# Optimization experiments

Hardware: AMD Instinct MI355X
Metric: run time of the kernel (lower is better)

The kernel has to match this reference:

```python
import jax, jax.numpy as jnp
import numpy as np

N = 50000          # num nodes
DEG = 16           # fixed degree (uniform CSR)
E = N * DEG        # num edges
R = 8              # num relations
IN = 128
HID = 128
OUT = 40
BN_EPS = 1e-5


def setup_inputs() -> dict:
    key = jax.random.key(0)
    k = jax.random.split(key, 5)
    x = jax.random.normal(k[0], (N, IN), jnp.float32)
    # glorot-ish init for per-relation weights
    W1 = jax.random.normal(k[1], (R, IN, HID), jnp.float32) * (2.0 / (IN + HID)) ** 0.5
    W2 = jax.random.normal(k[2], (R, HID, OUT), jnp.float32) * (2.0 / (HID + OUT)) ** 0.5
    ptr = jnp.arange(N + 1, dtype=jnp.int32) * DEG            # CSR row offsets
    idx = jax.random.randint(k[3], (E,), 0, N, jnp.int32)     # neighbor (src) ids
    edge_types = jax.random.randint(k[4], (E,), 0, R, jnp.int32)
    return {
        "x": x, "W1": W1, "W2": W2,
        "bn_gamma": jnp.ones((HID,), jnp.float32),
        "bn_beta": jnp.zeros((HID,), jnp.float32),
        "bn_mean": jnp.zeros((HID,), jnp.float32),
        "bn_var": jnp.ones((HID,), jnp.float32),
        "ptr": ptr, "idx": idx, "edge_types": edge_types,
    }


def _rgcn_layer(h, W, ptr, idx, edge_types):
    # RGCNOP: out[i] = sum_{e in [ptr[i],ptr[i+1])} x[idx[e]] @ W[etype[e]]
    # Efficient form: transform every node by every relation once, then gather
    # the (src, etype) pair per edge and scatter-add into destinations.
    xr = jnp.einsum('nd,rdh->nrh', h, W)             # [N, R, H]
    msgs = xr[idx, edge_types]                       # [E, H] irregular gather
    deg = ptr[1:] - ptr[:-1]                         # [N]
    dst = jnp.repeat(jnp.arange(ptr.shape[0] - 1, dtype=jnp.int32), deg,
                     total_repeat_length=idx.shape[0])
    agg = jax.ops.segment_sum(msgs, dst, num_segments=ptr.shape[0] - 1)
    return agg / deg[:, None].astype(agg.dtype)      # degree normalization


def reference(x, W1, W2, bn_gamma, bn_beta, bn_mean, bn_var, ptr, idx, edge_types):
    h = _rgcn_layer(x, W1, ptr, idx, edge_types)
    # BatchNorm1d in eval mode (history_size=0, dropout inactive)
    h = (h - bn_mean) * jax.lax.rsqrt(bn_var + BN_EPS) * bn_gamma + bn_beta
    h = jax.nn.relu(h)
    h = _rgcn_layer(h, W2, ptr, idx, edge_types)
    return jax.nn.log_softmax(h, axis=-1)
```

## Files before the change

### kernel.cpp

```cpp
#include <hip/hip_runtime.h>
#include <math.h>

typedef __attribute__((ext_vector_type(8))) short bf16x8;
typedef __attribute__((ext_vector_type(4))) float f32x4;

constexpr int kN   = 50000;
constexpr int kR   = 8;
constexpr int kIn  = 128;
constexpr int kHid = 128;
constexpr int kOut = 40;
constexpr int kNT  = 16;
constexpr int kLds = 1032;
constexpr float kBnEps = 1e-5f;

__device__ inline ushort f2bf(float x) {
    uint u = __float_as_uint(x);
    u += 0x7FFFu + ((u >> 16) & 1u);
    return (ushort)(u >> 16);
}
__device__ inline float bf2f(ushort s) { return __uint_as_float(((uint)s) << 16); }

__device__ __forceinline__ void pack_unit(const float* __restrict__ W,
                                          ushort* __restrict__ dst,
                                          int N, int frag, int lane)
{
    const int kt = frag & 31;
    const int nt = frag >> 5;
    const int n  = nt * 16 + (lane & 15);
    const int q  = lane >> 4;
    ushort hv[8];
    #pragma unroll
    for (int j = 0; j < 8; ++j) {
        const int k = kt * 32 + q * 8 + j;
        hv[j] = f2bf((n < N) ? W[(size_t)k * N + n] : 0.f);
    }
    const size_t o = ((size_t)frag * 64 + lane) * 8;
    *(ushort4*)&dst[o]     = make_ushort4(hv[0], hv[1], hv[2], hv[3]);
    *(ushort4*)&dst[o + 4] = make_ushort4(hv[4], hv[5], hv[6], hv[7]);
}

__global__ __launch_bounds__(256)
void prep(const float* __restrict__ x,  ushort* __restrict__ xb,
          const float* __restrict__ W1, ushort* __restrict__ W1hi,
          const float* __restrict__ W2, ushort* __restrict__ W2hi)
{
    const int b   = blockIdx.x;
    const int tid = threadIdx.x;
    if (b < 3125) {
        const size_t i = ((size_t)b * 256 + tid) * 8;
        const float4 v0 = *(const float4*)&x[i];
        const float4 v1 = *(const float4*)&x[i + 4];
        *(ushort4*)&xb[i]     = make_ushort4(f2bf(v0.x), f2bf(v0.y), f2bf(v0.z), f2bf(v0.w));
        *(ushort4*)&xb[i + 4] = make_ushort4(f2bf(v1.x), f2bf(v1.y), f2bf(v1.z), f2bf(v1.w));
    } else if (b < 3125 + 64) {
        pack_unit(W1, W1hi, kHid, (b - 3125) * 4 + (tid >> 6), tid & 63);
    } else {
        const int frag = (b - 3189) * 4 + (tid >> 6);
        if (frag < 96) pack_unit(W2, W2hi, kOut, frag, tid & 63);
    }
}

#define ACCUM_ET(ET, VX, VY)                                   \
    if      ((ET) == 0) { a0.x += (VX); a0.y += (VY); }        \
    else if ((ET) == 1) { a1.x += (VX); a1.y += (VY); }        \
    else if ((ET) == 2) { a2.x += (VX); a2.y += (VY); }        \
    else if ((ET) == 3) { a3.x += (VX); a3.y += (VY); }        \
    else if ((ET) == 4) { a4.x += (VX); a4.y += (VY); }        \
    else if ((ET) == 5) { a5.x += (VX); a5.y += (VY); }        \
    else if ((ET) == 6) { a6.x += (VX); a6.y += (VY); }        \
    else                { a7.x += (VX); a7.y += (VY); }

#define GATHER(BV, SRC) \
    const ushort2 BV = *(const ushort2*)&feat[(size_t)(SRC) * 128 + d2];

#define ACCUM_EDGE(J, BV) \
    { const int et = __builtin_amdgcn_readlane(ve, J); ACCUM_ET(et, bf2f(BV.x), bf2f(BV.y)) }

#define STORE_AGG(RR, AV) \
    *(ushort2*)&aggHi[n][(RR) * 128 + d2] = make_ushort2(f2bf(AV.x), f2bf(AV.y));

__device__ __forceinline__ void phaseA_bf16(const ushort* __restrict__ feat,
                                            const int* __restrict__ ptr,
                                            const int* __restrict__ idx,
                                            const int* __restrict__ etype,
                                            int base, ushort (*aggHi)[kLds])
{
    const int lane = threadIdx.x & 63;
    const int wid  = threadIdx.x >> 6;
    const int d2   = lane * 2;

    #pragma unroll
    for (int t = 0; t < 2; ++t) {
        const int n    = wid * 2 + t;
        const int node = base + n;
        const int p0   = ptr[node];
        const int deg  = ptr[node + 1] - p0;

        float2 a0 = {0.f,0.f}, a1 = {0.f,0.f}, a2 = {0.f,0.f}, a3 = {0.f,0.f};
        float2 a4 = {0.f,0.f}, a5 = {0.f,0.f}, a6 = {0.f,0.f}, a7 = {0.f,0.f};

        if (deg == 16) {
            const int vi = idx[p0 + (lane & 15)];
            const int ve = etype[p0 + (lane & 15)];
            const int s0  = __builtin_amdgcn_readlane(vi, 0);
            const int s1  = __builtin_amdgcn_readlane(vi, 1);
            const int s2  = __builtin_amdgcn_readlane(vi, 2);
            const int s3  = __builtin_amdgcn_readlane(vi, 3);
            const int s4  = __builtin_amdgcn_readlane(vi, 4);
            const int s5  = __builtin_amdgcn_readlane(vi, 5);
            const int s6  = __builtin_amdgcn_readlane(vi, 6);
            const int s7  = __builtin_amdgcn_readlane(vi, 7);
            const int s8  = __builtin_amdgcn_readlane(vi, 8);
            const int s9  = __builtin_amdgcn_readlane(vi, 9);
            const int s10 = __builtin_amdgcn_readlane(vi, 10);
            const int s11 = __builtin_amdgcn_readlane(vi, 11);
            const int s12 = __builtin_amdgcn_readlane(vi, 12);
            const int s13 = __builtin_amdgcn_readlane(vi, 13);
            const int s14 = __builtin_amdgcn_readlane(vi, 14);
            const int s15 = __builtin_amdgcn_readlane(vi, 15);
            GATHER(b0,  s0)  GATHER(b1,  s1)  GATHER(b2,  s2)  GATHER(b3,  s3)
            GATHER(b4,  s4)  GATHER(b5,  s5)  GATHER(b6,  s6)  GATHER(b7,  s7)
            GATHER(b8,  s8)  GATHER(b9,  s9)  GATHER(b10, s10) GATHER(b11, s11)
            GATHER(b12, s12) GATHER(b13, s13) GATHER(b14, s14) GATHER(b15, s15)
            ACCUM_EDGE(0,  b0)  ACCUM_EDGE(1,  b1)  ACCUM_EDGE(2,  b2)  ACCUM_EDGE(3,  b3)
            ACCUM_EDGE(4,  b4)  ACCUM_EDGE(5,  b5)  ACCUM_EDGE(6,  b6)  ACCUM_EDGE(7,  b7)
            ACCUM_EDGE(8,  b8)  ACCUM_EDGE(9,  b9)  ACCUM_EDGE(10, b10) ACCUM_EDGE(11, b11)
            ACCUM_EDGE(12, b12) ACCUM_EDGE(13, b13) ACCUM_EDGE(14, b14) ACCUM_EDGE(15, b15)
        } else {
            for (int e = p0; e < p0 + deg; ++e) {
                const int src = __builtin_amdgcn_readfirstlane(idx[e]);
                const int et  = __builtin_amdgcn_readfirstlane(etype[e]);
                const ushort2 u = *(const ushort2*)&feat[(size_t)src * 128 + d2];
                ACCUM_ET(et, bf2f(u.x), bf2f(u.y))
            }
        }
        STORE_AGG(0, a0) STORE_AGG(1, a1) STORE_AGG(2, a2) STORE_AGG(3, a3)
        STORE_AGG(4, a4) STORE_AGG(5, a5) STORE_AGG(6, a6) STORE_AGG(7, a7)
    }
}

__global__ __launch_bounds__(512, 4)
void rgcn_layer1(const ushort* __restrict__ xb,
                 const ushort* __restrict__ W1hi,
                 const float* __restrict__ gamma, const float* __restrict__ beta,
                 const float* __restrict__ mean,  const float* __restrict__ var,
                 const int* __restrict__ ptr, const int* __restrict__ idx,
                 const int* __restrict__ etype,
                 ushort* __restrict__ h1b)
{
    __shared__ ushort aggHi[kNT][kLds];
    const int tid  = threadIdx.x;
    const int base = blockIdx.x * kNT;

    phaseA_bf16(xb, ptr, idx, etype, base, aggHi);
    __syncthreads();

    const int lane = tid & 63;
    const int wid  = tid >> 6;
    const int m    = lane & 15;
    const int q    = lane >> 4;

    const bf16x8* Bh = (const bf16x8*)W1hi + (size_t)wid * 32 * 64 + lane;
    f32x4 acc = {0.f, 0.f, 0.f, 0.f};

    #pragma unroll 4
    for (int kt = 0; kt < 32; ++kt) {
        const bf16x8 ah = *(const bf16x8*)&aggHi[m][kt * 32 + q * 8];
        const bf16x8 bh = Bh[(size_t)kt * 64];
        acc = __builtin_amdgcn_mfma_f32_16x16x32_bf16(ah, bh, acc, 0, 0, 0);
    }

    const int c = wid * 16 + m;
    const float g  = gamma[c] * rsqrtf(var[c] + kBnEps);
    const float mu = mean[c];
    const float bt = beta[c];
    #pragma unroll
    for (int i = 0; i < 4; ++i) {
        const int node = base + q * 4 + i;
        const float invdeg = 1.0f / (float)(ptr[node + 1] - ptr[node]);
        float v = (acc[i] * invdeg - mu) * g + bt;
        v = fmaxf(v, 0.f);
        h1b[(size_t)node * kHid + c] = f2bf(v);
    }
}

__global__ __launch_bounds__(512, 4)
void rgcn_layer2(const ushort* __restrict__ h1b,
                 const ushort* __restrict__ W2hi,
                 const int* __restrict__ ptr, const int* __restrict__ idx,
                 const int* __restrict__ etype,
                 float* __restrict__ out)
{
    __shared__ ushort aggHi[kNT][kLds];
    __shared__ float logits[kNT][48];
    const int tid  = threadIdx.x;
    const int base = blockIdx.x * kNT;

    phaseA_bf16(h1b, ptr, idx, etype, base, aggHi);
    __syncthreads();

    const int lane = tid & 63;
    const int wid  = tid >> 6;
    const int m    = lane & 15;
    const int q    = lane >> 4;

    if (wid < 3) {
        const bf16x8* Bh = (const bf16x8*)W2hi + (size_t)wid * 32 * 64 + lane;
        f32x4 acc = {0.f, 0.f, 0.f, 0.f};
        #pragma unroll 4
        for (int kt = 0; kt < 32; ++kt) {
            const bf16x8 ah = *(const bf16x8*)&aggHi[m][kt * 32 + q * 8];
            const bf16x8 bh = Bh[(size_t)kt * 64];
            acc = __builtin_amdgcn_mfma_f32_16x16x32_bf16(ah, bh, acc, 0, 0, 0);
        }
        const int n = wid * 16 + m;
        if (n < kOut) {
            #pragma unroll
            for (int i = 0; i < 4; ++i) {
                const int node = base + q * 4 + i;
                const float invdeg = 1.0f / (float)(ptr[node + 1] - ptr[node]);
                logits[q * 4 + i][n] = acc[i] * invdeg;
            }
        }
    }
    __syncthreads();

    #pragma unroll
    for (int i = 0; i < 2; ++i) {
        const int nrow = wid * 2 + i;
        const int node = base + nrow;
        const float v = (lane < kOut) ? logits[nrow][lane] : -INFINITY;
        float mx = v;
        #pragma unroll
        for (int off = 32; off > 0; off >>= 1)
            mx = fmaxf(mx, __shfl_xor(mx, off, 64));
        float s = (lane < kOut) ? __expf(v - mx) : 0.f;
        #pragma unroll
        for (int off = 32; off > 0; off >>= 1)
            s += __shfl_xor(s, off, 64);
        if (lane < kOut)
            out[(size_t)node * kOut + lane] = v - mx - __logf(s);
    }
}

extern "C" void kernel_launch(void* const* d_in, const int* in_sizes, int n_in,
                              void* d_out, int out_size, void* d_ws, size_t ws_size,
                              hipStream_t stream)
{
    const float* x     = (const float*)d_in[0];
    const float* W1    = (const float*)d_in[1];
    const float* W2    = (const float*)d_in[2];
    const float* gamma = (const float*)d_in[3];
    const float* beta  = (const float*)d_in[4];
    const float* mean  = (const float*)d_in[5];
    const float* var   = (const float*)d_in[6];
    const int*   ptr   = (const int*)d_in[7];
    const int*   idx   = (const int*)d_in[8];
    const int*   et    = (const int*)d_in[9];
    float*       out   = (float*)d_out;

    char* ws = (char*)d_ws;
    ushort* h1b  = (ushort*)ws;
    ushort* xb   = (ushort*)(ws + 12800000);
    ushort* W1hi = (ushort*)(ws + 25600000);
    ushort* W2hi = (ushort*)(ws + 25600000 + 262144);

    prep<<<dim3(3125 + 64 + 24), dim3(256), 0, stream>>>(x, xb, W1, W1hi, W2, W2hi);

    dim3 grid(kN / kNT), block(512);
    rgcn_layer1<<<grid, block, 0, stream>>>(xb, W1hi, gamma, beta, mean, var,
                                            ptr, idx, et, h1b);
    rgcn_layer2<<<grid, block, 0, stream>>>(h1b, W2hi, ptr, idx, et, out);
}
```

Baseline: 197.3 us.

## Issue both nodes' neighbor gathers together and use hardware bf16 pack conversion

```diff
diff --git a/kernel.cpp b/kernel.cpp
--- a/kernel.cpp
+++ b/kernel.cpp
@@ -13,12 +13,13 @@
 constexpr int kLds = 1032;
 constexpr float kBnEps = 1e-5f;
 
-__device__ inline ushort f2bf(float x) {
-    uint u = __float_as_uint(x);
-    u += 0x7FFFu + ((u >> 16) & 1u);
-    return (ushort)(u >> 16);
-}
 __device__ inline float bf2f(ushort s) { return __uint_as_float(((uint)s) << 16); }
+
+__device__ __forceinline__ uint cvtpk(float a, float b) {
+    uint r;
+    asm("v_cvt_pk_bf16_f32 %0, %1, %2" : "=v"(r) : "v"(a), "v"(b));
+    return r;
+}
 
 __device__ __forceinline__ void pack_unit(const float* __restrict__ W,
                                           ushort* __restrict__ dst,
@@ -28,15 +29,15 @@
     const int nt = frag >> 5;
     const int n  = nt * 16 + (lane & 15);
     const int q  = lane >> 4;
-    ushort hv[8];
+    float f[8];
     #pragma unroll
     for (int j = 0; j < 8; ++j) {
         const int k = kt * 32 + q * 8 + j;
-        hv[j] = f2bf((n < N) ? W[(size_t)k * N + n] : 0.f);
+        f[j] = (n < N) ? W[(size_t)k * N + n] : 0.f;
     }
     const size_t o = ((size_t)frag * 64 + lane) * 8;
-    *(ushort4*)&dst[o]     = make_ushort4(hv[0], hv[1], hv[2], hv[3]);
-    *(ushort4*)&dst[o + 4] = make_ushort4(hv[4], hv[5], hv[6], hv[7]);
+    *(uint4*)&dst[o] = make_uint4(cvtpk(f[0], f[1]), cvtpk(f[2], f[3]),
+                                  cvtpk(f[4], f[5]), cvtpk(f[6], f[7]));
 }
 
 __global__ __launch_bounds__(256)
@@ -50,8 +51,8 @@
         const size_t i = ((size_t)b * 256 + tid) * 8;
         const float4 v0 = *(const float4*)&x[i];
         const float4 v1 = *(const float4*)&x[i + 4];
-        *(ushort4*)&xb[i]     = make_ushort4(f2bf(v0.x), f2bf(v0.y), f2bf(v0.z), f2bf(v0.w));
-        *(ushort4*)&xb[i + 4] = make_ushort4(f2bf(v1.x), f2bf(v1.y), f2bf(v1.z), f2bf(v1.w));
+        *(uint4*)&xb[i] = make_uint4(cvtpk(v0.x, v0.y), cvtpk(v0.z, v0.w),
+                                     cvtpk(v1.x, v1.y), cvtpk(v1.z, v1.w));
     } else if (b < 3125 + 64) {
         pack_unit(W1, W1hi, kHid, (b - 3125) * 4 + (tid >> 6), tid & 63);
     } else {
@@ -60,24 +61,55 @@
     }
 }
 
-#define ACCUM_ET(ET, VX, VY)                                   \
-    if      ((ET) == 0) { a0.x += (VX); a0.y += (VY); }        \
-    else if ((ET) == 1) { a1.x += (VX); a1.y += (VY); }        \
-    else if ((ET) == 2) { a2.x += (VX); a2.y += (VY); }        \
-    else if ((ET) == 3) { a3.x += (VX); a3.y += (VY); }        \
-    else if ((ET) == 4) { a4.x += (VX); a4.y += (VY); }        \
-    else if ((ET) == 5) { a5.x += (VX); a5.y += (VY); }        \
-    else if ((ET) == 6) { a6.x += (VX); a6.y += (VY); }        \
-    else                { a7.x += (VX); a7.y += (VY); }
-
-#define GATHER(BV, SRC) \
-    const ushort2 BV = *(const ushort2*)&feat[(size_t)(SRC) * 128 + d2];
-
-#define ACCUM_EDGE(J, BV) \
-    { const int et = __builtin_amdgcn_readlane(ve, J); ACCUM_ET(et, bf2f(BV.x), bf2f(BV.y)) }
-
-#define STORE_AGG(RR, AV) \
-    *(ushort2*)&aggHi[n][(RR) * 128 + d2] = make_ushort2(f2bf(AV.x), f2bf(AV.y));
+#define ACCUM_ET(ET, VX, VY)                                                   \
+    if ((ET) < 4) {                                                            \
+        if ((ET) < 2) {                                                        \
+            if ((ET) == 0) { a0.x += (VX); a0.y += (VY); }                     \
+            else           { a1.x += (VX); a1.y += (VY); }                     \
+        } else {                                                               \
+            if ((ET) == 2) { a2.x += (VX); a2.y += (VY); }                     \
+            else           { a3.x += (VX); a3.y += (VY); }                     \
+        }                                                                      \
+    } else {                                                                   \
+        if ((ET) < 6) {                                                        \
+            if ((ET) == 4) { a4.x += (VX); a4.y += (VY); }                     \
+            else           { a5.x += (VX); a5.y += (VY); }                     \
+        } else {                                                               \
+            if ((ET) == 6) { a6.x += (VX); a6.y += (VY); }                     \
+            else           { a7.x += (VX); a7.y += (VY); }                     \
+        }                                                                      \
+    }
+
+#define RD(V, J) __builtin_amdgcn_readlane((V), (J))
+
+#define G(BV, VI, J)                                                           \
+    const ushort2 BV = *(const ushort2*)&feat[(size_t)RD(VI, J) * 128 + d2];
+
+#define ACCUM_EDGE(VE, J, BV)                                                  \
+    { const int et = RD(VE, J);                                                \
+      const float vx = bf2f(BV.x), vy = bf2f(BV.y);                            \
+      ACCUM_ET(et, vx, vy) }
+
+#define ZERO_ACC                                                               \
+    float2 a0 = {0.f,0.f}, a1 = {0.f,0.f}, a2 = {0.f,0.f}, a3 = {0.f,0.f};     \
+    float2 a4 = {0.f,0.f}, a5 = {0.f,0.f}, a6 = {0.f,0.f}, a7 = {0.f,0.f};
+
+#define STORE8(NN)                                                             \
+    { const int nloc = (NN);                                                   \
+      *(uint*)&aggHi[nloc][0 * 128 + d2] = cvtpk(a0.x, a0.y);                  \
+      *(uint*)&aggHi[nloc][1 * 128 + d2] = cvtpk(a1.x, a1.y);                  \
+      *(uint*)&aggHi[nloc][2 * 128 + d2] = cvtpk(a2.x, a2.y);                  \
+      *(uint*)&aggHi[nloc][3 * 128 + d2] = cvtpk(a3.x, a3.y);                  \
+      *(uint*)&aggHi[nloc][4 * 128 + d2] = cvtpk(a4.x, a4.y);                  \
+      *(uint*)&aggHi[nloc][5 * 128 + d2] = cvtpk(a5.x, a5.y);                  \
+      *(uint*)&aggHi[nloc][6 * 128 + d2] = cvtpk(a6.x, a6.y);                  \
+      *(uint*)&aggHi[nloc][7 * 128 + d2] = cvtpk(a7.x, a7.y); }
+
+#define KEEP16(B0,B1,B2,B3,B4,B5,B6,B7,B8,B9,B10,B11,B12,B13,B14,B15)          \
+    asm volatile("" :: "v"(B0),"v"(B1),"v"(B2),"v"(B3),                        \
+                       "v"(B4),"v"(B5),"v"(B6),"v"(B7),                        \
+                       "v"(B8),"v"(B9),"v"(B10),"v"(B11),                      \
+                       "v"(B12),"v"(B13),"v"(B14),"v"(B15));
 
 __device__ __forceinline__ void phaseA_bf16(const ushort* __restrict__ feat,
                                             const int* __restrict__ ptr,
@@ -89,53 +121,69 @@
     const int wid  = threadIdx.x >> 6;
     const int d2   = lane * 2;
 
-    #pragma unroll
-    for (int t = 0; t < 2; ++t) {
-        const int n    = wid * 2 + t;
-        const int node = base + n;
-        const int p0   = ptr[node];
-        const int deg  = ptr[node + 1] - p0;
-
-        float2 a0 = {0.f,0.f}, a1 = {0.f,0.f}, a2 = {0.f,0.f}, a3 = {0.f,0.f};
-        float2 a4 = {0.f,0.f}, a5 = {0.f,0.f}, a6 = {0.f,0.f}, a7 = {0.f,0.f};
-
-        if (deg == 16) {
-            const int vi = idx[p0 + (lane & 15)];
-            const int ve = etype[p0 + (lane & 15)];
-            const int s0  = __builtin_amdgcn_readlane(vi, 0);
-            const int s1  = __builtin_amdgcn_readlane(vi, 1);
-            const int s2  = __builtin_amdgcn_readlane(vi, 2);
-            const int s3  = __builtin_amdgcn_readlane(vi, 3);
-            const int s4  = __builtin_amdgcn_readlane(vi, 4);
-            const int s5  = __builtin_amdgcn_readlane(vi, 5);
-            const int s6  = __builtin_amdgcn_readlane(vi, 6);
-            const int s7  = __builtin_amdgcn_readlane(vi, 7);
-            const int s8  = __builtin_amdgcn_readlane(vi, 8);
-            const int s9  = __builtin_amdgcn_readlane(vi, 9);
-            const int s10 = __builtin_amdgcn_readlane(vi, 10);
-            const int s11 = __builtin_amdgcn_readlane(vi, 11);
-            const int s12 = __builtin_amdgcn_readlane(vi, 12);
-            const int s13 = __builtin_amdgcn_readlane(vi, 13);
-            const int s14 = __builtin_amdgcn_readlane(vi, 14);
-            const int s15 = __builtin_amdgcn_readlane(vi, 15);
-            GATHER(b0,  s0)  GATHER(b1,  s1)  GATHER(b2,  s2)  GATHER(b3,  s3)
-            GATHER(b4,  s4)  GATHER(b5,  s5)  GATHER(b6,  s6)  GATHER(b7,  s7)
-            GATHER(b8,  s8)  GATHER(b9,  s9)  GATHER(b10, s10) GATHER(b11, s11)
-            GATHER(b12, s12) GATHER(b13, s13) GATHER(b14, s14) GATHER(b15, s15)
-            ACCUM_EDGE(0,  b0)  ACCUM_EDGE(1,  b1)  ACCUM_EDGE(2,  b2)  ACCUM_EDGE(3,  b3)
-            ACCUM_EDGE(4,  b4)  ACCUM_EDGE(5,  b5)  ACCUM_EDGE(6,  b6)  ACCUM_EDGE(7,  b7)
-            ACCUM_EDGE(8,  b8)  ACCUM_EDGE(9,  b9)  ACCUM_EDGE(10, b10) ACCUM_EDGE(11, b11)
-            ACCUM_EDGE(12, b12) ACCUM_EDGE(13, b13) ACCUM_EDGE(14, b14) ACCUM_EDGE(15, b15)
-        } else {
-            for (int e = p0; e < p0 + deg; ++e) {
+    const int node0 = base + wid * 2;
+    const int p0 = ptr[node0];
+    const int p1 = ptr[node0 + 1];
+    const int p2 = ptr[node0 + 2];
+
+    if (((p1 - p0) == 16) & ((p2 - p1) == 16)) {
+        const int vi0 = idx[p0 + (lane & 15)];
+        const int ve0 = etype[p0 + (lane & 15)];
+        const int vi1 = idx[p1 + (lane & 15)];
+        const int ve1 = etype[p1 + (lane & 15)];
+
+        G(b0,  vi0, 0)  G(b1,  vi0, 1)  G(b2,  vi0, 2)  G(b3,  vi0, 3)
+        G(b4,  vi0, 4)  G(b5,  vi0, 5)  G(b6,  vi0, 6)  G(b7,  vi0, 7)
+        G(b8,  vi0, 8)  G(b9,  vi0, 9)  G(b10, vi0, 10) G(b11, vi0, 11)
+        G(b12, vi0, 12) G(b13, vi0, 13) G(b14, vi0, 14) G(b15, vi0, 15)
+        G(c0,  vi1, 0)  G(c1,  vi1, 1)  G(c2,  vi1, 2)  G(c3,  vi1, 3)
+        G(c4,  vi1, 4)  G(c5,  vi1, 5)  G(c6,  vi1, 6)  G(c7,  vi1, 7)
+        G(c8,  vi1, 8)  G(c9,  vi1, 9)  G(c10, vi1, 10) G(c11, vi1, 11)
+        G(c12, vi1, 12) G(c13, vi1, 13) G(c14, vi1, 14) G(c15, vi1, 15)
+
+        KEEP16(b0,b1,b2,b3,b4,b5,b6,b7,b8,b9,b10,b11,b12,b13,b14,b15)
+        KEEP16(c0,c1,c2,c3,c4,c5,c6,c7,c8,c9,c10,c11,c12,c13,c14,c15)
+
+        {
+            ZERO_ACC
+            ACCUM_EDGE(ve0, 0,  b0)  ACCUM_EDGE(ve0, 1,  b1)
+            ACCUM_EDGE(ve0, 2,  b2)  ACCUM_EDGE(ve0, 3,  b3)
+            ACCUM_EDGE(ve0, 4,  b4)  ACCUM_EDGE(ve0, 5,  b5)
+            ACCUM_EDGE(ve0, 6,  b6)  ACCUM_EDGE(ve0, 7,  b7)
+            ACCUM_EDGE(ve0, 8,  b8)  ACCUM_EDGE(ve0, 9,  b9)
+            ACCUM_EDGE(ve0, 10, b10) ACCUM_EDGE(ve0, 11, b11)
+            ACCUM_EDGE(ve0, 12, b12) ACCUM_EDGE(ve0, 13, b13)
+            ACCUM_EDGE(ve0, 14, b14) ACCUM_EDGE(ve0, 15, b15)
+            STORE8(wid * 2)
+        }
+        {
+            ZERO_ACC
+            ACCUM_EDGE(ve1, 0,  c0)  ACCUM_EDGE(ve1, 1,  c1)
+            ACCUM_EDGE(ve1, 2,  c2)  ACCUM_EDGE(ve1, 3,  c3)
+            ACCUM_EDGE(ve1, 4,  c4)  ACCUM_EDGE(ve1, 5,  c5)
+            ACCUM_EDGE(ve1, 6,  c6)  ACCUM_EDGE(ve1, 7,  c7)
+            ACCUM_EDGE(ve1, 8,  c8)  ACCUM_EDGE(ve1, 9,  c9)
+            ACCUM_EDGE(ve1, 10, c10) ACCUM_EDGE(ve1, 11, c11)
+            ACCUM_EDGE(ve1, 12, c12) ACCUM_EDGE(ve1, 13, c13)
+            ACCUM_EDGE(ve1, 14, c14) ACCUM_EDGE(ve1, 15, c15)
+            STORE8(wid * 2 + 1)
+        }
+    } else {
+        #pragma unroll
+        for (int t = 0; t < 2; ++t) {
+            const int node = node0 + t;
+            const int pa   = ptr[node];
+            const int deg  = ptr[node + 1] - pa;
+            ZERO_ACC
+            for (int e = pa; e < pa + deg; ++e) {
                 const int src = __builtin_amdgcn_readfirstlane(idx[e]);
                 const int et  = __builtin_amdgcn_readfirstlane(etype[e]);
                 const ushort2 u = *(const ushort2*)&feat[(size_t)src * 128 + d2];
-                ACCUM_ET(et, bf2f(u.x), bf2f(u.y))
+                const float vx = bf2f(u.x), vy = bf2f(u.y);
+                ACCUM_ET(et, vx, vy)
             }
-        }
-        STORE_AGG(0, a0) STORE_AGG(1, a1) STORE_AGG(2, a2) STORE_AGG(3, a3)
-        STORE_AGG(4, a4) STORE_AGG(5, a5) STORE_AGG(6, a6) STORE_AGG(7, a7)
+            STORE8(wid * 2 + t)
+        }
     }
 }
 
@@ -174,14 +222,20 @@
     const float g  = gamma[c] * rsqrtf(var[c] + kBnEps);
     const float mu = mean[c];
     const float bt = beta[c];
+    float v[4];
     #pragma unroll
     for (int i = 0; i < 4; ++i) {
         const int node = base + q * 4 + i;
         const float invdeg = 1.0f / (float)(ptr[node + 1] - ptr[node]);
-        float v = (acc[i] * invdeg - mu) * g + bt;
-        v = fmaxf(v, 0.f);
-        h1b[(size_t)node * kHid + c] = f2bf(v);
-    }
+        v[i] = fmaxf((acc[i] * invdeg - mu) * g + bt, 0.f);
+    }
+    const uint p01 = cvtpk(v[0], v[1]);
+    const uint p23 = cvtpk(v[2], v[3]);
+    const int n0 = base + q * 4;
+    h1b[(size_t)(n0 + 0) * kHid + c] = (ushort)(p01 & 0xFFFFu);
+    h1b[(size_t)(n0 + 1) * kHid + c] = (ushort)(p01 >> 16);
+    h1b[(size_t)(n0 + 2) * kHid + c] = (ushort)(p23 & 0xFFFFu);
+    h1b[(size_t)(n0 + 3) * kHid + c] = (ushort)(p23 >> 16);
 }
 
 __global__ __launch_bounds__(512, 4)
```

Result: slower. 216.7 us (+9.8%).
